# Performance work log

Hardware: AMD Instinct MI355X
Metric: run time of the kernel (lower is better)

## Reference

```python
import jax, jax.numpy as jnp
import numpy as np


def setup_inputs() -> dict:
    key = jax.random.key(0)
    ks = jax.random.split(key, 7)
    B, C, H, W = 16, 256, 64, 64
    s = 1.0 / np.sqrt(C)  # ~kaiming-uniform scale for 1x1 conv
    return {
        "a": jax.random.normal(ks[0], (B, C, H, W), jnp.float32),
        "wq": jax.random.normal(ks[1], (C, C), jnp.float32) * s,
        "bq": jax.random.normal(ks[2], (C,), jnp.float32) * s,
        "wk": jax.random.normal(ks[3], (C, C), jnp.float32) * s,
        "bk": jax.random.normal(ks[4], (C,), jnp.float32) * s,
        "wv": jax.random.normal(ks[5], (C, C), jnp.float32) * s,
        "bv": jax.random.normal(ks[6], (C,), jnp.float32) * s,
    }


def reference(a, wq, bq, wk, bk, wv, bv):
    # 1x1 conv == per-pixel linear: [B,C,H,W] x [O,C] -> [B,H,W,O]
    def proj(w, b):
        return jnp.einsum('bchw,oc->bhwo', a, w) + b

    q = proj(wq, bq)  # [B,H,W,C]
    k = proj(wk, bk)
    v = proj(wv, bv)

    # unnormalized dot-product attention over the W axis, per row H
    attn = jnp.einsum('bhwc,bhxc->bhwx', q, k)       # [B,H,W,W]
    att_out = jnp.einsum('bhwx,bhxc->bhwc', attn, v)  # [B,H,W,C]

    # permute back to NCHW and residual add
    return a + jnp.transpose(att_out, (0, 3, 1, 2))
```

## Files before the change

### kernel.cpp

```cpp
#include <hip/hip_runtime.h>
#include <hip/hip_bf16.h>

#define NB 16
#define NC 256
#define NH 64
#define NW 64

typedef __attribute__((ext_vector_type(8))) short bf16x8;
typedef __attribute__((ext_vector_type(4))) float f32x4;

__device__ __forceinline__ unsigned short f2bf(float f) {
    union { float f; unsigned int u; } v; v.f = f;
    unsigned int u = v.u;
    u += 0x7fffu + ((u >> 16) & 1u);
    return (unsigned short)(u >> 16);
}

__device__ __forceinline__ int swzT(int row, int col) {
    return row * 256 + ((((col >> 3) ^ (row & 7) ^ ((row >> 3) & 7)) << 3) | (col & 7));
}
__device__ __forceinline__ int swzS(int row, int col) {
    return row * 64 + ((((col >> 3) ^ (row & 7) ^ ((row >> 3) & 7)) << 3) | (col & 7));
}

__global__ void prep_g(const float* __restrict__ wq, const float* __restrict__ wk,
                       const float* __restrict__ bq, const float* __restrict__ bk,
                       unsigned short* __restrict__ wsb) {
    int c2 = threadIdx.x;
    int c1 = blockIdx.x;
    if (c1 < 256) {
        float acc = 0.f;
        #pragma unroll 4
        for (int o = 0; o < 256; ++o)
            acc += wq[o * 256 + c1] * wk[o * 256 + c2];
        wsb[c1 * 256 + c2] = f2bf(acc);
    } else {
        float u = 0.f, v = 0.f;
        #pragma unroll 4
        for (int o = 0; o < 256; ++o) {
            u += bq[o] * wk[o * 256 + c2];
            v += bk[o] * wq[o * 256 + c2];
        }
        wsb[131072 + c2] = f2bf(u);
        wsb[131328 + c2] = f2bf(v);
        if (c2 == 0) {
            float s = 0.f;
            for (int o = 0; o < 256; ++o) s += bq[o] * bk[o];
            *(float*)(wsb + 131584) = s;
        }
    }
}

__global__ void prep_wv(const float* __restrict__ wv, unsigned short* __restrict__ wsb) {
    int i = blockIdx.x * 256 + threadIdx.x;
    float4 t = ((const float4*)wv)[i];
    ushort4 u = { f2bf(t.x), f2bf(t.y), f2bf(t.z), f2bf(t.w) };
    ((ushort4*)(wsb + 65536))[i] = u;
}

__launch_bounds__(512, 4)
__global__ void mha_fused(const float* __restrict__ a,
                          const unsigned short* __restrict__ wsb,
                          const float* __restrict__ bv,
                          float* __restrict__ out) {
    __shared__ __align__(16) unsigned short smem[36864];
    __shared__ __align__(16) float uAvA[128];
    unsigned short* AT  = smem;
    unsigned short* TT  = smem + 16384;
    unsigned short* Vs  = smem + 16384;
    unsigned short* ATT = smem + 32768;

    const unsigned short* Gb  = wsb;
    const unsigned short* Wvb = wsb + 65536;
    const unsigned short* ub  = wsb + 131072;
    const unsigned short* vbv = wsb + 131328;

    const int tid = threadIdx.x;
    const int b = blockIdx.x >> 6;
    const int h = blockIdx.x & 63;
    const float* aB = a + (size_t)b * (NC * NH * NW) + h * NW;

    #pragma unroll
    for (int half = 0; half < 2; ++half) {
        int mt = tid + half * 512;
        int c0 = (mt >> 4) << 2;
        int w0 = (mt & 15) << 2;
        float4 r0 = *(const float4*)(aB + (size_t)(c0 + 0) * 4096 + w0);
        float4 r1 = *(const float4*)(aB + (size_t)(c0 + 1) * 4096 + w0);
        float4 r2 = *(const float4*)(aB + (size_t)(c0 + 2) * 4096 + w0);
        float4 r3 = *(const float4*)(aB + (size_t)(c0 + 3) * 4096 + w0);
        const float* f0 = (const float*)&r0;
        const float* f1 = (const float*)&r1;
        const float* f2 = (const float*)&r2;
        const float* f3 = (const float*)&r3;
        #pragma unroll
        for (int j = 0; j < 4; ++j) {
            ushort4 u = { f2bf(f0[j]), f2bf(f1[j]), f2bf(f2[j]), f2bf(f3[j]) };
            *(ushort4*)(AT + swzT(w0 + j, c0)) = u;
        }
    }
    __syncthreads();

    const int wv_ = tid >> 6;
    const int lane = tid & 63;
    const int l15 = lane & 15;
    const int g = lane >> 4;

    {
        f32x4 acc[2][4];
        #pragma unroll
        for (int mi = 0; mi < 2; ++mi)
            #pragma unroll
            for (int n = 0; n < 4; ++n) acc[mi][n] = { 0.f, 0.f, 0.f, 0.f };

        const bool is_u = (wv_ < 4);
        const int uvtile = wv_ & 3;
        const int uvrow = uvtile * 16 + l15;
        const float sval = *(const float*)(wsb + 131584);
        f32x4 accu;
        #pragma unroll
        for (int r = 0; r < 4; ++r) accu[r] = is_u ? sval : 0.f;
        const unsigned short* uvp = is_u ? ub : vbv;

        #pragma unroll
        for (int kk = 0; kk < 8; ++kk) {
            bf16x8 gf[2], atf[4];
            #pragma unroll
            for (int mi = 0; mi < 2; ++mi)
                gf[mi] = *(const bf16x8*)(Gb + (wv_ * 32 + mi * 16 + l15) * 256 + kk * 32 + g * 8);
            #pragma unroll
            for (int n = 0; n < 4; ++n)
                atf[n] = *(const bf16x8*)(AT + swzT(n * 16 + l15, kk * 32 + g * 8));
            #pragma unroll
            for (int mi = 0; mi < 2; ++mi)
                #pragma unroll
                for (int n = 0; n < 4; ++n)
                    acc[mi][n] = __builtin_amdgcn_mfma_f32_16x16x32_bf16(gf[mi], atf[n], acc[mi][n], 0, 0, 0);
            bf16x8 uvf  = *(const bf16x8*)(uvp + kk * 32 + g * 8);
            bf16x8 uvbf = *(const bf16x8*)(AT + swzT(uvrow, kk * 32 + g * 8));
            accu = __builtin_amdgcn_mfma_f32_16x16x32_bf16(uvf, uvbf, accu, 0, 0, 0);
        }
        #pragma unroll
        for (int mi = 0; mi < 2; ++mi) {
            int c1_0 = wv_ * 32 + mi * 16 + g * 4;
            #pragma unroll
            for (int n = 0; n < 4; ++n) {
                ushort4 u = { f2bf(acc[mi][n][0]), f2bf(acc[mi][n][1]),
                              f2bf(acc[mi][n][2]), f2bf(acc[mi][n][3]) };
                *(ushort4*)(TT + swzT(n * 16 + l15, c1_0)) = u;
            }
        }
        if (g == 0)
            uAvA[(is_u ? 0 : 64) + uvrow] = accu[0];
    }
    __syncthreads();

    const int wt3 = wv_ >> 1;
    const int xb3 = (wv_ & 1) * 2;
    {
        f32x4 acc3[2] = { { 0, 0, 0, 0 }, { 0, 0, 0, 0 } };
        #pragma unroll
        for (int kk = 0; kk < 8; ++kk) {
            bf16x8 awf = *(const bf16x8*)(AT + swzT(wt3 * 16 + l15, kk * 32 + g * 8));
            #pragma unroll
            for (int j = 0; j < 2; ++j) {
                bf16x8 txf = *(const bf16x8*)(TT + swzT((xb3 + j) * 16 + l15, kk * 32 + g * 8));
                acc3[j] = __builtin_amdgcn_mfma_f32_16x16x32_bf16(txf, awf, acc3[j], 0, 0, 0);
            }
        }
        const int w = wt3 * 16 + l15;
        const float vAw = uAvA[64 + w];
        #pragma unroll
        for (int j = 0; j < 2; ++j) {
            int x0 = (xb3 + j) * 16 + g * 4;
            float4 uq = *(const float4*)&uAvA[x0];
            const float* uqa = (const float*)&uq;
            ushort4 u = { f2bf(acc3[j][0] + uqa[0] + vAw), f2bf(acc3[j][1] + uqa[1] + vAw),
                          f2bf(acc3[j][2] + uqa[2] + vAw), f2bf(acc3[j][3] + uqa[3] + vAw) };
            *(ushort4*)(ATT + swzS(w, x0)) = u;
        }
    }
    __syncthreads();

    {
        f32x4 acc[2][4];
        #pragma unroll
        for (int mi = 0; mi < 2; ++mi) {
            float bvl = bv[wv_ * 32 + mi * 16 + l15];
            #pragma unroll
            for (int n = 0; n < 4; ++n) acc[mi][n] = { bvl, bvl, bvl, bvl };
        }
        #pragma unroll
        for (int kk = 0; kk < 8; ++kk) {
            bf16x8 atx[4], wvf[2];
            #pragma unroll
            for (int n = 0; n < 4; ++n)
                atx[n] = *(const bf16x8*)(AT + swzT(n * 16 + l15, kk * 32 + g * 8));
            #pragma unroll
            for (int mi = 0; mi < 2; ++mi)
                wvf[mi] = *(const bf16x8*)(Wvb + (wv_ * 32 + mi * 16 + l15) * 256 + kk * 32 + g * 8);
            #pragma unroll
            for (int mi = 0; mi < 2; ++mi)
                #pragma unroll
                for (int n = 0; n < 4; ++n)
                    acc[mi][n] = __builtin_amdgcn_mfma_f32_16x16x32_bf16(atx[n], wvf[mi], acc[mi][n], 0, 0, 0);
        }
        #pragma unroll
        for (int mi = 0; mi < 2; ++mi) {
            int c = wv_ * 32 + mi * 16 + l15;
            #pragma unroll
            for (int n = 0; n < 4; ++n) {
                ushort4 u = { f2bf(acc[mi][n][0]), f2bf(acc[mi][n][1]),
                              f2bf(acc[mi][n][2]), f2bf(acc[mi][n][3]) };
                *(ushort4*)(Vs + swzS(c, n * 16 + g * 4)) = u;
            }
        }
    }
    __syncthreads();

    {
        f32x4 acc[2][4];
        #pragma unroll
        for (int mi = 0; mi < 2; ++mi)
            #pragma unroll
            for (int n = 0; n < 4; ++n) acc[mi][n] = { 0.f, 0.f, 0.f, 0.f };
        #pragma unroll
        for (int kk = 0; kk < 2; ++kk) {
            bf16x8 attf[4], vsf[2];
            #pragma unroll
            for (int n = 0; n < 4; ++n)
                attf[n] = *(const bf16x8*)(ATT + swzS(n * 16 + l15, kk * 32 + g * 8));
            #pragma unroll
            for (int mi = 0; mi < 2; ++mi)
                vsf[mi] = *(const bf16x8*)(Vs + swzS(wv_ * 32 + mi * 16 + l15, kk * 32 + g * 8));
            #pragma unroll
            for (int mi = 0; mi < 2; ++mi)
                #pragma unroll
                for (int n = 0; n < 4; ++n)
                    acc[mi][n] = __builtin_amdgcn_mfma_f32_16x16x32_bf16(attf[n], vsf[mi], acc[mi][n], 0, 0, 0);
        }
        float* outB = out + (size_t)b * (NC * NH * NW) + h * NW;
        #pragma unroll
        for (int mi = 0; mi < 2; ++mi) {
            int c = wv_ * 32 + mi * 16 + l15;
            const float* ain = aB + (size_t)c * 4096;
            float* po = outB + (size_t)c * 4096;
            #pragma unroll
            for (int n = 0; n < 4; ++n) {
                int w0 = n * 16 + g * 4;
                float4 res = *(const float4*)(ain + w0);
                float4 o4;
                o4.x = res.x + acc[mi][n][0];
                o4.y = res.y + acc[mi][n][1];
                o4.z = res.z + acc[mi][n][2];
                o4.w = res.w + acc[mi][n][3];
                *(float4*)(po + w0) = o4;
            }
        }
    }
}

extern "C" void kernel_launch(void* const* d_in, const int* in_sizes, int n_in,
                              void* d_out, int out_size, void* d_ws, size_t ws_size,
                              hipStream_t stream) {
    (void)in_sizes; (void)n_in; (void)out_size; (void)ws_size;
    const float* a  = (const float*)d_in[0];
    const float* wq = (const float*)d_in[1];
    const float* bq = (const float*)d_in[2];
    const float* wk = (const float*)d_in[3];
    const float* bk = (const float*)d_in[4];
    const float* wv = (const float*)d_in[5];
    const float* bv = (const float*)d_in[6];
    float* out = (float*)d_out;
    unsigned short* wsb = (unsigned short*)d_ws;

    prep_g<<<dim3(257), dim3(256), 0, stream>>>(wq, wk, bq, bk, wsb);
    prep_wv<<<dim3(64), dim3(256), 0, stream>>>(wv, wsb);
    mha_fused<<<dim3(NB * NH), dim3(512), 0, stream>>>(a, wsb, bv, out);
}
```

Baseline: 95.76 us.

## Merge prep kernels and software-prefetch global weight fragments in fused attention

Merges the two weight-preparation kernels into one launch. The Wq^T*Wk product is computed with 8 outputs per thread, cutting blocks from 256 to 32. In the fused kernel, the G and Wv global fragment loads are double-buffered one k-step ahead so they overlap the MFMA work. The residual input is loaded before the V projection rather than in the epilogue, so its latency hides behind compute. The trade-off is higher register pressure under launch_bounds(512,4), which may cause spills, and fewer blocks in the prep kernel.

```diff
diff --git a/kernel.cpp b/kernel.cpp
--- a/kernel.cpp
+++ b/kernel.cpp
@@ -23,39 +23,44 @@
     return row * 64 + ((((col >> 3) ^ (row & 7) ^ ((row >> 3) & 7)) << 3) | (col & 7));
 }
 
-__global__ void prep_g(const float* __restrict__ wq, const float* __restrict__ wk,
-                       const float* __restrict__ bq, const float* __restrict__ bk,
-                       unsigned short* __restrict__ wsb) {
-    int c2 = threadIdx.x;
-    int c1 = blockIdx.x;
-    if (c1 < 256) {
-        float acc = 0.f;
-        #pragma unroll 4
-        for (int o = 0; o < 256; ++o)
-            acc += wq[o * 256 + c1] * wk[o * 256 + c2];
-        wsb[c1 * 256 + c2] = f2bf(acc);
+__global__ void prep(const float* __restrict__ wq, const float* __restrict__ wk,
+                     const float* __restrict__ wv,
+                     const float* __restrict__ bq, const float* __restrict__ bk,
+                     unsigned short* __restrict__ wsb) {
+    int bx = blockIdx.x;
+    int t = threadIdx.x;
+    if (bx < 64) {
+        int i = bx * 256 + t;
+        float4 v4 = ((const float4*)wv)[i];
+        ushort4 u = { f2bf(v4.x), f2bf(v4.y), f2bf(v4.z), f2bf(v4.w) };
+        ((ushort4*)(wsb + 65536))[i] = u;
+    } else if (bx < 96) {
+        int c1_0 = (bx - 64) * 8;
+        float acc[8] = {0.f, 0.f, 0.f, 0.f, 0.f, 0.f, 0.f, 0.f};
+        for (int o = 0; o < 256; ++o) {
+            float wkv = wk[o * 256 + t];
+            #pragma unroll
+            for (int i = 0; i < 8; ++i)
+                acc[i] += wq[o * 256 + c1_0 + i] * wkv;
+        }
+        #pragma unroll
+        for (int i = 0; i < 8; ++i)
+            wsb[(c1_0 + i) * 256 + t] = f2bf(acc[i]);
     } else {
         float u = 0.f, v = 0.f;
         #pragma unroll 4
         for (int o = 0; o < 256; ++o) {
-            u += bq[o] * wk[o * 256 + c2];
-            v += bk[o] * wq[o * 256 + c2];
-        }
-        wsb[131072 + c2] = f2bf(u);
-        wsb[131328 + c2] = f2bf(v);
-        if (c2 == 0) {
+            u += bq[o] * wk[o * 256 + t];
+            v += bk[o] * wq[o * 256 + t];
+        }
+        wsb[131072 + t] = f2bf(u);
+        wsb[131328 + t] = f2bf(v);
+        if (t == 0) {
             float s = 0.f;
             for (int o = 0; o < 256; ++o) s += bq[o] * bk[o];
             *(float*)(wsb + 131584) = s;
         }
     }
-}
-
-__global__ void prep_wv(const float* __restrict__ wv, unsigned short* __restrict__ wsb) {
-    int i = blockIdx.x * 256 + threadIdx.x;
-    float4 t = ((const float4*)wv)[i];
-    ushort4 u = { f2bf(t.x), f2bf(t.y), f2bf(t.z), f2bf(t.w) };
-    ((ushort4*)(wsb + 65536))[i] = u;
 }
 
 __launch_bounds__(512, 4)
@@ -114,31 +119,39 @@
             for (int n = 0; n < 4; ++n) acc[mi][n] = { 0.f, 0.f, 0.f, 0.f };
 
         const bool is_u = (wv_ < 4);
-        const int uvtile = wv_ & 3;
-        const int uvrow = uvtile * 16 + l15;
+        const int uvrow = (wv_ & 3) * 16 + l15;
         const float sval = *(const float*)(wsb + 131584);
         f32x4 accu;
         #pragma unroll
         for (int r = 0; r < 4; ++r) accu[r] = is_u ? sval : 0.f;
         const unsigned short* uvp = is_u ? ub : vbv;
 
+        const unsigned short* g0p = Gb + (wv_ * 32 + l15) * 256 + g * 8;
+        const unsigned short* g1p = Gb + (wv_ * 32 + 16 + l15) * 256 + g * 8;
+        bf16x8 gf0 = *(const bf16x8*)(g0p);
+        bf16x8 gf1 = *(const bf16x8*)(g1p);
+        bf16x8 uvf = *(const bf16x8*)(uvp + g * 8);
+
         #pragma unroll
         for (int kk = 0; kk < 8; ++kk) {
-            bf16x8 gf[2], atf[4];
-            #pragma unroll
-            for (int mi = 0; mi < 2; ++mi)
-                gf[mi] = *(const bf16x8*)(Gb + (wv_ * 32 + mi * 16 + l15) * 256 + kk * 32 + g * 8);
+            bf16x8 cg0 = gf0, cg1 = gf1, cuv = uvf;
+            if (kk < 7) {
+                gf0 = *(const bf16x8*)(g0p + (kk + 1) * 32);
+                gf1 = *(const bf16x8*)(g1p + (kk + 1) * 32);
+                uvf = *(const bf16x8*)(uvp + (kk + 1) * 32 + g * 8);
+            }
+            bf16x8 atf[4];
             #pragma unroll
             for (int n = 0; n < 4; ++n)
                 atf[n] = *(const bf16x8*)(AT + swzT(n * 16 + l15, kk * 32 + g * 8));
-            #pragma unroll
-            for (int mi = 0; mi < 2; ++mi)
-                #pragma unroll
-                for (int n = 0; n < 4; ++n)
-                    acc[mi][n] = __builtin_amdgcn_mfma_f32_16x16x32_bf16(gf[mi], atf[n], acc[mi][n], 0, 0, 0);
-            bf16x8 uvf  = *(const bf16x8*)(uvp + kk * 32 + g * 8);
             bf16x8 uvbf = *(const bf16x8*)(AT + swzT(uvrow, kk * 32 + g * 8));
-            accu = __builtin_amdgcn_mfma_f32_16x16x32_bf16(uvf, uvbf, accu, 0, 0, 0);
+            #pragma unroll
+            for (int n = 0; n < 4; ++n)
+                acc[0][n] = __builtin_amdgcn_mfma_f32_16x16x32_bf16(cg0, atf[n], acc[0][n], 0, 0, 0);
+            #pragma unroll
+            for (int n = 0; n < 4; ++n)
+                acc[1][n] = __builtin_amdgcn_mfma_f32_16x16x32_bf16(cg1, atf[n], acc[1][n], 0, 0, 0);
+            accu = __builtin_amdgcn_mfma_f32_16x16x32_bf16(cuv, uvbf, accu, 0, 0, 0);
         }
         #pragma unroll
         for (int mi = 0; mi < 2; ++mi) {
@@ -182,6 +195,14 @@
     }
     __syncthreads();
 
+    float4 res[2][4];
+    #pragma unroll
+    for (int mi = 0; mi < 2; ++mi) {
+        int c = wv_ * 32 + mi * 16 + l15;
+        #pragma unroll
+        for (int n = 0; n < 4; ++n)
+            res[mi][n] = *(const float4*)(aB + (size_t)c * 4096 + n * 16 + g * 4);
+    }
     {
         f32x4 acc[2][4];
         #pragma unroll
@@ -190,20 +211,27 @@
             #pragma unroll
             for (int n = 0; n < 4; ++n) acc[mi][n] = { bvl, bvl, bvl, bvl };
         }
+        const unsigned short* w0p = Wvb + (wv_ * 32 + l15) * 256 + g * 8;
+        const unsigned short* w1p = Wvb + (wv_ * 32 + 16 + l15) * 256 + g * 8;
+        bf16x8 wf0 = *(const bf16x8*)(w0p);
+        bf16x8 wf1 = *(const bf16x8*)(w1p);
         #pragma unroll
         for (int kk = 0; kk < 8; ++kk) {
-            bf16x8 atx[4], wvf[2];
+            bf16x8 cw0 = wf0, cw1 = wf1;
+            if (kk < 7) {
+                wf0 = *(const bf16x8*)(w0p + (kk + 1) * 32);
+                wf1 = *(const bf16x8*)(w1p + (kk + 1) * 32);
+            }
+            bf16x8 atx[4];
             #pragma unroll
             for (int n = 0; n < 4; ++n)
                 atx[n] = *(const bf16x8*)(AT + swzT(n * 16 + l15, kk * 32 + g * 8));
             #pragma unroll
-            for (int mi = 0; mi < 2; ++mi)
-                wvf[mi] = *(const bf16x8*)(Wvb + (wv_ * 32 + mi * 16 + l15) * 256 + kk * 32 + g * 8);
-            #pragma unroll
-            for (int mi = 0; mi < 2; ++mi)
-                #pragma unroll
-                for (int n = 0; n < 4; ++n)
-                    acc[mi][n] = __builtin_amdgcn_mfma_f32_16x16x32_bf16(atx[n], wvf[mi], acc[mi][n], 0, 0, 0);
+            for (int n = 0; n < 4; ++n)
+                acc[0][n] = __builtin_amdgcn_mfma_f32_16x16x32_bf16(atx[n], cw0, acc[0][n], 0, 0, 0);
+            #pragma unroll
+            for (int n = 0; n < 4; ++n)
+                acc[1][n] = __builtin_amdgcn_mfma_f32_16x16x32_bf16(atx[n], cw1, acc[1][n], 0, 0, 0);
         }
         #pragma unroll
         for (int mi = 0; mi < 2; ++mi) {
@@ -243,17 +271,15 @@
         #pragma unroll
         for (int mi = 0; mi < 2; ++mi) {
             int c = wv_ * 32 + mi * 16 + l15;
-            const float* ain = aB + (size_t)c * 4096;
             float* po = outB + (size_t)c * 4096;
             #pragma unroll
             for (int n = 0; n < 4; ++n) {
                 int w0 = n * 16 + g * 4;
-                float4 res = *(const float4*)(ain + w0);
                 float4 o4;
-                o4.x = res.x + acc[mi][n][0];
-                o4.y = res.y + acc[mi][n][1];
-                o4.z = res.z + acc[mi][n][2];
-                o4.w = res.w + acc[mi][n][3];
+                o4.x = res[mi][n].x + acc[mi][n][0];
+                o4.y = res[mi][n].y + acc[mi][n][1];
+                o4.z = res[mi][n].z + acc[mi][n][2];
+                o4.w = res[mi][n].w + acc[mi][n][3];
                 *(float4*)(po + w0) = o4;
             }
         }
@@ -274,7 +300,6 @@
     float* out = (float*)d_out;
     unsigned short* wsb = (unsigned short*)d_ws;
 
-    prep_g<<<dim3(257), dim3(256), 0, stream>>>(wq, wk, bq, bk, wsb);
-    prep_wv<<<dim3(64), dim3(256), 0, stream>>>(wv, wsb);
+    prep<<<dim3(97), dim3(256), 0, stream>>>(wq, wk, wv, bq, bk, wsb);
     mha_fused<<<dim3(NB * NH), dim3(512), 0, stream>>>(a, wsb, bv, out);
 }
```

Measured after the change: 94.86 us. Within noise of the previous version (-0.9%).
